# Kernel tuning notes

Measured on AMD Instinct MI355X. Metric: run time of the kernel, lower is better.

Reference implementation:

```python
import jax, jax.numpy as jnp
import numpy as np

IN_DIM, MEM_DIM, NUM_WORDS, N_LEAVES = 300, 256, 50000, 8192


def setup_inputs() -> dict:
    key = jax.random.key(0)
    ks = jax.random.split(key, 6)
    s = 0.05
    return {
        "embs": jax.random.normal(ks[0], (N_LEAVES, IN_DIM), jnp.float32),
        "Wx": jax.random.normal(ks[1], (4 * MEM_DIM, IN_DIM), jnp.float32) * s,
        "bx": jax.random.normal(ks[2], (4 * MEM_DIM,), jnp.float32) * s,
        "Wl": jax.random.normal(ks[3], (5 * MEM_DIM, MEM_DIM), jnp.float32) * s,
        "Wr": jax.random.normal(ks[4], (5 * MEM_DIM, MEM_DIM), jnp.float32) * s,
        "emb_table": jax.random.normal(ks[5], (NUM_WORDS, IN_DIM), jnp.float32),
    }


def reference(embs, Wx, bx, Wl, Wr, emb_table):
    m = Wl.shape[1]

    # x-projection order along fused axis: [cx, ix, fx, ox]
    def proj_x(x):  # [B, in] -> [B, 4, m]
        return (x @ Wx.T + bx).reshape(x.shape[0], 4, m)

    # hidden-projection order: [u, i, lf, rf, o]
    def compose(xg, lc, lh, rc, rh):
        lg = (lh @ Wl.T).reshape(-1, 5, m)
        rg = (rh @ Wr.T).reshape(-1, 5, m)
        u = jnp.tanh(xg[:, 0] + lg[:, 0] + rg[:, 0])
        i = jax.nn.sigmoid(xg[:, 1] + lg[:, 1] + rg[:, 1])
        lf = jax.nn.sigmoid(xg[:, 2] + lg[:, 2] + rg[:, 2])  # fx shared
        rf = jax.nn.sigmoid(xg[:, 2] + lg[:, 3] + rg[:, 3])  # fx shared
        c = i * u + lf * lc + rf * rc
        o = jax.nn.sigmoid(xg[:, 3] + lg[:, 4] + rg[:, 4])
        h = o * jnp.tanh(c)
        return c, h

    # leaves: zero child states, per-leaf embedding inputs
    L = embs.shape[0]
    z = jnp.zeros((L, m), embs.dtype)
    c, h = compose(proj_x(embs), z, z, z, z)

    # internal nodes (PAD=True): input is word_embedding(num_words - 1)
    pad_xg = proj_x(emb_table[-1:])  # [1, 4, m]

    while c.shape[0] > 1:  # static shapes; 13 merge levels
        lc, rc = c[0::2], c[1::2]
        lh, rh = h[0::2], h[1::2]
        B = lc.shape[0]
        c, h = compose(jnp.broadcast_to(pad_xg, (B, 4, m)), lc, lh, rc, rh)

    return jnp.stack([c, h])  # root (c, h): [2, 1, mem_dim]
```

## Files before the change

### kernel.cpp

```cpp
#include <hip/hip_runtime.h>
#include <math.h>


#define MEM 256

typedef __attribute__((ext_vector_type(8))) short bf16x8;
typedef __attribute__((ext_vector_type(4))) float f32x4;

__device__ __forceinline__ float sigf(float x) { return 1.0f / (1.0f + __expf(-x)); }

__device__ __forceinline__ unsigned short f2b(float f) {
  unsigned int u = __float_as_uint(f);
  u = (u + 0x7FFFu + ((u >> 16) & 1u)) >> 16;
  return (unsigned short)u;
}

__device__ __forceinline__ bf16x8 c8(const float* __restrict__ p) {
  float4 f0 = *(const float4*)(p);
  float4 f1 = *(const float4*)(p + 4);
  bf16x8 r;
  r[0] = (short)f2b(f0.x); r[1] = (short)f2b(f0.y);
  r[2] = (short)f2b(f0.z); r[3] = (short)f2b(f0.w);
  r[4] = (short)f2b(f1.x); r[5] = (short)f2b(f1.y);
  r[6] = (short)f2b(f1.z); r[7] = (short)f2b(f1.w);
  return r;
}

__device__ __forceinline__ bf16x8 g8(const float* __restrict__ rp, int k0) {
  if (k0 + 8 <= 300) return c8(rp + k0);
  bf16x8 r;
#pragma unroll
  for (int j = 0; j < 8; j++) {
    int k = k0 + j;
    r[j] = (k < 300) ? (short)f2b(rp[k]) : (short)0;
  }
  return r;
}

#define NB_EB 1280
#define NB_WCF 320
#define NB_WXF 120
__global__ __launch_bounds__(256) void k_prep(
    const float* __restrict__ embs, const float* __restrict__ Wx,
    const float* __restrict__ bx, const float* __restrict__ Wl,
    const float* __restrict__ Wr, const float* __restrict__ emb_last,
    unsigned short* __restrict__ eb, unsigned short* __restrict__ Wcf,
    unsigned short* __restrict__ Wxf, float* __restrict__ bias5) {
  int b = blockIdx.x, tid = threadIdx.x;
  if (b < NB_EB) {
    int idx8 = (b * 256 + tid) * 8;
    int row = idx8 / 320;
    int k0 = idx8 - row * 320;
    *(bf16x8*)(eb + idx8) = g8(embs + row * 300, k0);
  } else if (b < NB_EB + NB_WCF) {
    int idx8 = ((b - NB_EB) * 256 + tid) * 8;
    int f = idx8 >> 9, rr = idx8 & 511;
    int lane = rr >> 3;
    int gate = f % 5, t = f / 5;
    int grp = t & 15, kc = t >> 4;
    int k0 = kc * 32 + ((lane >> 4) << 3);
    int n = gate * 256 + (grp << 4) + (lane & 15);
    const float* src = (k0 < 256) ? (Wl + n * 256 + k0) : (Wr + n * 256 + (k0 - 256));
    *(bf16x8*)(Wcf + idx8) = c8(src);
  } else if (b < NB_EB + NB_WCF + NB_WXF) {
    int idx8 = ((b - NB_EB - NB_WCF) * 256 + tid) * 8;
    int f = idx8 >> 9, rr = idx8 & 511;
    int lane = rr >> 3;
    int gate = f % 3, t = f / 3;
    int grp = t & 15, kc = t >> 4;
    int k0 = kc * 32 + ((lane >> 4) << 3);
    const int gmap[3] = {0, 1, 3};
    int n = gmap[gate] * 256 + (grp << 4) + (lane & 15);
    *(bf16x8*)(Wxf + idx8) = g8(Wx + n * 300, k0);
  } else {
    int g = b - (NB_EB + NB_WCF + NB_WXF);
    __shared__ float er[300];
    for (int k = tid; k < 300; k += 256) er[k] = emb_last[k];
    __syncthreads();
    const int map[5] = {0, 1, 2, 2, 3};
    int wrow = map[g] * 256 + tid;
    const float* w = Wx + wrow * 300;
    float s = bx[wrow];
    for (int k = 0; k < 300; k++) s += er[k] * w[k];
    bias5[g * 256 + tid] = s;
  }
}

__global__ __launch_bounds__(256) void k_leaf_mfma(
    const unsigned short* __restrict__ eb, const unsigned short* __restrict__ Wxf,
    const float* __restrict__ bx, float* __restrict__ cO,
    unsigned short* __restrict__ hO) {
  int bid = blockIdx.x;
  int slice = bid & 7, rest = bid >> 3;
  int rowblock = slice * 8 + (rest & 7);
  int grp = rest >> 3;
  int lane = threadIdx.x & 63;
  int wave = threadIdx.x >> 6;
  int tb = (rowblock * 4 + wave) * 2;
  int m = lane & 15, quad = lane >> 4;

  f32x4 acc[2][3];
#pragma unroll
  for (int rt = 0; rt < 2; rt++)
#pragma unroll
    for (int g = 0; g < 3; g++) acc[rt][g] = (f32x4){0.f, 0.f, 0.f, 0.f};

  const unsigned short* ar0 = eb + (tb * 16 + m) * 320 + quad * 8;
  const unsigned short* ar1 = eb + ((tb + 1) * 16 + m) * 320 + quad * 8;
#pragma unroll
  for (int kc = 0; kc < 10; kc++) {
    const unsigned short* bp = Wxf + ((kc * 16 + grp) * 3) * 512 + lane * 8;
    bf16x8 b0 = *(const bf16x8*)(bp);
    bf16x8 b1 = *(const bf16x8*)(bp + 512);
    bf16x8 b2 = *(const bf16x8*)(bp + 1024);
    bf16x8 a0 = *(const bf16x8*)(ar0 + kc * 32);
    bf16x8 a1 = *(const bf16x8*)(ar1 + kc * 32);
    acc[0][0] = __builtin_amdgcn_mfma_f32_16x16x32_bf16(a0, b0, acc[0][0], 0, 0, 0);
    acc[0][1] = __builtin_amdgcn_mfma_f32_16x16x32_bf16(a0, b1, acc[0][1], 0, 0, 0);
    acc[0][2] = __builtin_amdgcn_mfma_f32_16x16x32_bf16(a0, b2, acc[0][2], 0, 0, 0);
    acc[1][0] = __builtin_amdgcn_mfma_f32_16x16x32_bf16(a1, b0, acc[1][0], 0, 0, 0);
    acc[1][1] = __builtin_amdgcn_mfma_f32_16x16x32_bf16(a1, b1, acc[1][1], 0, 0, 0);
    acc[1][2] = __builtin_amdgcn_mfma_f32_16x16x32_bf16(a1, b2, acc[1][2], 0, 0, 0);
  }
  int col = grp * 16 + m;
  float b0 = bx[col], b1 = bx[256 + col], b3 = bx[768 + col];
#pragma unroll
  for (int rt = 0; rt < 2; rt++) {
#pragma unroll
    for (int reg = 0; reg < 4; reg++) {
      int row = (tb + rt) * 16 + quad * 4 + reg;
      float u = tanhf(acc[rt][0][reg] + b0);
      float ig = sigf(acc[rt][1][reg] + b1);
      float o = sigf(acc[rt][2][reg] + b3);
      float c = ig * u;
      cO[row * MEM + col] = c;
      hO[row * MEM + col] = f2b(o * tanhf(c));
    }
  }
}

template <int RT>
__global__ __launch_bounds__(256) void k_compose_mfma(
    const unsigned short* __restrict__ hprev,
    const float* __restrict__ cprev,
    const unsigned short* __restrict__ Wcf, const float* __restrict__ bias5,
    float* __restrict__ cO, unsigned short* __restrict__ hO,
    float* __restrict__ hOf, int B) {
  int tiles = B >> 4;
  int gx = tiles / (4 * RT);
  int S = gx >= 8 ? 8 : gx;
  int pc = gx / S;
  int bid = blockIdx.x;
  int slice = bid % S;
  int rest = bid / S;
  int rowblock = slice * pc + rest % pc;
  int grp = rest / pc;
  int lane = threadIdx.x & 63;
  int wave = threadIdx.x >> 6;
  int tb = (rowblock * 4 + wave) * RT;
  if (tb * 16 >= B) return;
  int m = lane & 15, quad = lane >> 4;
  const bf16x8 zz = {0, 0, 0, 0, 0, 0, 0, 0};

  f32x4 acc[RT][5];
  const unsigned short* ar[RT];
  bool ok[RT];
#pragma unroll
  for (int rt = 0; rt < RT; rt++) {
    int ra = (tb + rt) * 16 + m;
    ok[rt] = (ra < B);
    ar[rt] = hprev + ra * 512 + quad * 8;
#pragma unroll
    for (int g = 0; g < 5; g++) acc[rt][g] = (f32x4){0.f, 0.f, 0.f, 0.f};
  }

#pragma unroll
  for (int kc = 0; kc < 16; kc++) {
    const unsigned short* bp = Wcf + ((kc * 16 + grp) * 5) * 512 + lane * 8;
    bf16x8 b0 = *(const bf16x8*)(bp);
    bf16x8 b1 = *(const bf16x8*)(bp + 512);
    bf16x8 b2 = *(const bf16x8*)(bp + 1024);
    bf16x8 b3 = *(const bf16x8*)(bp + 1536);
    bf16x8 b4 = *(const bf16x8*)(bp + 2048);
#pragma unroll
    for (int rt = 0; rt < RT; rt++) {
      bf16x8 a = ok[rt] ? *(const bf16x8*)(ar[rt] + kc * 32) : zz;
      acc[rt][0] = __builtin_amdgcn_mfma_f32_16x16x32_bf16(a, b0, acc[rt][0], 0, 0, 0);
      acc[rt][1] = __builtin_amdgcn_mfma_f32_16x16x32_bf16(a, b1, acc[rt][1], 0, 0, 0);
      acc[rt][2] = __builtin_amdgcn_mfma_f32_16x16x32_bf16(a, b2, acc[rt][2], 0, 0, 0);
      acc[rt][3] = __builtin_amdgcn_mfma_f32_16x16x32_bf16(a, b3, acc[rt][3], 0, 0, 0);
      acc[rt][4] = __builtin_amdgcn_mfma_f32_16x16x32_bf16(a, b4, acc[rt][4], 0, 0, 0);
    }
  }
  int col = grp * 16 + m;
  float b0 = bias5[col], b1 = bias5[256 + col], b2 = bias5[512 + col];
  float b3 = bias5[768 + col], b4 = bias5[1024 + col];
#pragma unroll
  for (int rt = 0; rt < RT; rt++) {
#pragma unroll
    for (int reg = 0; reg < 4; reg++) {
      int row = (tb + rt) * 16 + quad * 4 + reg;
      if (row >= B) continue;
      float u = tanhf(acc[rt][0][reg] + b0);
      float ig = sigf(acc[rt][1][reg] + b1);
      float lf = sigf(acc[rt][2][reg] + b2);
      float rf = sigf(acc[rt][3][reg] + b3);
      float o = sigf(acc[rt][4][reg] + b4);
      float lc = cprev[(2 * row) * MEM + col];
      float rc = cprev[(2 * row + 1) * MEM + col];
      float c = ig * u + lf * lc + rf * rc;
      float h = o * tanhf(c);
      cO[row * MEM + col] = c;
      hO[row * MEM + col] = f2b(h);
      if (hOf) hOf[row * MEM + col] = h;
    }
  }
}

__global__ __launch_bounds__(256) void k_compose_ksplit(
    const unsigned short* __restrict__ hprev, const float* __restrict__ cprev,
    const unsigned short* __restrict__ Wcf, const float* __restrict__ bias5,
    float* __restrict__ cO, unsigned short* __restrict__ hO,
    float* __restrict__ hOf, int B) {
  __shared__ __align__(16) float lds[4 * 2 * 5 * 64 * 4];
  int tid = threadIdx.x;
  int lane = tid & 63, wave = tid >> 6;
  int grp = blockIdx.y;
  int m = lane & 15, quad = lane >> 4;
  int tiles = (B + 15) >> 4;
  const bf16x8 zz = {0, 0, 0, 0, 0, 0, 0, 0};

  f32x4 acc[2][5];
  bool ok[2];
  const unsigned short* ar[2];
#pragma unroll
  for (int t = 0; t < 2; t++) {
    int ra = t * 16 + m;
    ok[t] = (t < tiles) && (ra < B);
    ar[t] = hprev + ra * 512 + quad * 8;
#pragma unroll
    for (int q = 0; q < 5; q++) acc[t][q] = (f32x4){0.f, 0.f, 0.f, 0.f};
  }

#pragma unroll
  for (int kcl = 0; kcl < 4; kcl++) {
    int kc = wave * 4 + kcl;
    const unsigned short* bp = Wcf + ((kc * 16 + grp) * 5) * 512 + lane * 8;
    bf16x8 b0 = *(const bf16x8*)(bp);
    bf16x8 b1 = *(const bf16x8*)(bp + 512);
    bf16x8 b2 = *(const bf16x8*)(bp + 1024);
    bf16x8 b3 = *(const bf16x8*)(bp + 1536);
    bf16x8 b4 = *(const bf16x8*)(bp + 2048);
#pragma unroll
    for (int t = 0; t < 2; t++) {
      if (t < tiles) {
        bf16x8 a = ok[t] ? *(const bf16x8*)(ar[t] + kc * 32) : zz;
        acc[t][0] = __builtin_amdgcn_mfma_f32_16x16x32_bf16(a, b0, acc[t][0], 0, 0, 0);
        acc[t][1] = __builtin_amdgcn_mfma_f32_16x16x32_bf16(a, b1, acc[t][1], 0, 0, 0);
        acc[t][2] = __builtin_amdgcn_mfma_f32_16x16x32_bf16(a, b2, acc[t][2], 0, 0, 0);
        acc[t][3] = __builtin_amdgcn_mfma_f32_16x16x32_bf16(a, b3, acc[t][3], 0, 0, 0);
        acc[t][4] = __builtin_amdgcn_mfma_f32_16x16x32_bf16(a, b4, acc[t][4], 0, 0, 0);
      }
    }
  }
#pragma unroll
  for (int t = 0; t < 2; t++)
    if (t < tiles)
#pragma unroll
      for (int q = 0; q < 5; q++)
        *(f32x4*)&lds[(((wave * 2 + t) * 5 + q) * 64 + lane) * 4] = acc[t][q];
  __syncthreads();

  if (wave < tiles) {
    int t = wave;
    int col = grp * 16 + m;
    float b0 = bias5[col], b1 = bias5[256 + col], b2 = bias5[512 + col];
    float b3 = bias5[768 + col], b4 = bias5[1024 + col];
    f32x4 s[5];
#pragma unroll
    for (int q = 0; q < 5; q++) {
      s[q] = *(const f32x4*)&lds[(((0 * 2 + t) * 5 + q) * 64 + lane) * 4];
#pragma unroll
      for (int v = 1; v < 4; v++) {
        f32x4 p = *(const f32x4*)&lds[(((v * 2 + t) * 5 + q) * 64 + lane) * 4];
        s[q][0] += p[0]; s[q][1] += p[1]; s[q][2] += p[2]; s[q][3] += p[3];
      }
    }
#pragma unroll
    for (int reg = 0; reg < 4; reg++) {
      int row = t * 16 + quad * 4 + reg;
      if (row >= B) continue;
      float u = tanhf(s[0][reg] + b0);
      float ig = sigf(s[1][reg] + b1);
      float lf = sigf(s[2][reg] + b2);
      float rf = sigf(s[3][reg] + b3);
      float o = sigf(s[4][reg] + b4);
      float lc = cprev[(2 * row) * MEM + col];
      float rc = cprev[(2 * row + 1) * MEM + col];
      float c = ig * u + lf * lc + rf * rc;
      float h = o * tanhf(c);
      cO[row * MEM + col] = c;
      hO[row * MEM + col] = f2b(h);
      if (hOf) hOf[row * MEM + col] = h;
    }
  }
}

extern "C" void kernel_launch(void* const* d_in, const int* in_sizes, int n_in,
                              void* d_out, int out_size, void* d_ws, size_t ws_size,
                              hipStream_t stream) {
  const float* embs = (const float*)d_in[0];
  const float* Wx = (const float*)d_in[1];
  const float* bx = (const float*)d_in[2];
  const float* Wl = (const float*)d_in[3];
  const float* Wr = (const float*)d_in[4];
  const float* emb_table = (const float*)d_in[5];
  float* out = (float*)d_out;

  float* ws = (float*)d_ws;
  float* cA = ws;
  float* cB = cA + 8192 * 256;
  float* bias5 = cB + 4096 * 256;
  unsigned short* hA = (unsigned short*)(bias5 + 1280);
  unsigned short* hB = hA + 8192 * 256;
  unsigned short* Wcf = hB + 4096 * 256;
  unsigned short* Wxf = Wcf + 1280 * 512;
  unsigned short* eb = Wxf + 480 * 512;

  k_prep<<<NB_EB + NB_WCF + NB_WXF + 5, 256, 0, stream>>>(
      embs, Wx, bx, Wl, Wr, emb_table + (in_sizes[5] - 300),
      eb, Wcf, Wxf, bias5);

  k_leaf_mfma<<<1024, 256, 0, stream>>>(eb, Wxf, bx, cA, hA);

  const float* cs = cA;
  const unsigned short* hs = hA;
  int B = 4096;
  int lvl = 0;
  while (B >= 1) {
    float* dc;
    unsigned short* dh;
    float* dhf = nullptr;
    if (B == 1) {
      dc = out;
      dh = hB;
      dhf = out + 256;
    } else if ((lvl & 1) == 0) {
      dc = cB; dh = hB;
    } else {
      dc = cA; dh = hA;
    }
    if (B == 4096) {
      int gx = (B >> 4) / 8;
      k_compose_mfma<2><<<gx * 16, 256, 0, stream>>>(
          hs, cs, Wcf, bias5, dc, dh, dhf, B);
    } else if (B >= 64) {
      int gx = (B >> 4) / 4;
      k_compose_mfma<1><<<gx * 16, 256, 0, stream>>>(
          hs, cs, Wcf, bias5, dc, dh, dhf, B);
    } else {
      k_compose_ksplit<<<dim3(1, 16), 256, 0, stream>>>(
          hs, cs, Wcf, bias5, dc, dh, dhf, B);
    }
    cs = dc;
    hs = dh;
    B >>= 1;
    lvl++;
  }
}
```

Measured before the change: 249.3 us.

## Fuse weight prep into leaf kernel and use K-split compose for all upper levels

Splits prep so that only the embedding and Wx conversion run before the leaf kernel. Wcf packing and the pad bias are moved into extra blocks of the leaf kernel, where they run alongside the leaf MFMA work. Every level from B=2048 down now uses the K-split compose kernel, with the A fragments preloaded into registers and tiles spread across blockIdx.x. This gives each block a quarter of K and so more blocks per level, at the cost of an LDS reduction step. The first level gets a dedicated RT=2 kernel with the bounds checks removed.

```diff
diff --git a/kernel.cpp b/kernel.cpp
--- a/kernel.cpp
+++ b/kernel.cpp
@@ -38,22 +38,87 @@
 }
 
 #define NB_EB 1280
-#define NB_WCF 320
 #define NB_WXF 120
-__global__ __launch_bounds__(256) void k_prep(
+__global__ __launch_bounds__(256) void k_prep1(
     const float* __restrict__ embs, const float* __restrict__ Wx,
-    const float* __restrict__ bx, const float* __restrict__ Wl,
-    const float* __restrict__ Wr, const float* __restrict__ emb_last,
-    unsigned short* __restrict__ eb, unsigned short* __restrict__ Wcf,
-    unsigned short* __restrict__ Wxf, float* __restrict__ bias5) {
+    unsigned short* __restrict__ eb, unsigned short* __restrict__ Wxf) {
   int b = blockIdx.x, tid = threadIdx.x;
   if (b < NB_EB) {
     int idx8 = (b * 256 + tid) * 8;
     int row = idx8 / 320;
     int k0 = idx8 - row * 320;
     *(bf16x8*)(eb + idx8) = g8(embs + row * 300, k0);
-  } else if (b < NB_EB + NB_WCF) {
+  } else {
     int idx8 = ((b - NB_EB) * 256 + tid) * 8;
+    int f = idx8 >> 9, rr = idx8 & 511;
+    int lane = rr >> 3;
+    int gate = f % 3, t = f / 3;
+    int grp = t & 15, kc = t >> 4;
+    int k0 = kc * 32 + ((lane >> 4) << 3);
+    const int gmap[3] = {0, 1, 3};
+    int n = gmap[gate] * 256 + (grp << 4) + (lane & 15);
+    *(bf16x8*)(Wxf + idx8) = g8(Wx + n * 300, k0);
+  }
+}
+
+#define NB_LEAF 1024
+#define NB_WCF 320
+__global__ __launch_bounds__(256) void k_leaf_fused(
+    const unsigned short* __restrict__ eb, const unsigned short* __restrict__ Wxf,
+    const float* __restrict__ bx, const float* __restrict__ Wx,
+    const float* __restrict__ Wl, const float* __restrict__ Wr,
+    const float* __restrict__ emb_last,
+    unsigned short* __restrict__ Wcf, float* __restrict__ bias5,
+    float* __restrict__ cO, unsigned short* __restrict__ hO) {
+  int b = blockIdx.x, tid = threadIdx.x;
+  if (b < NB_LEAF) {
+    int slice = b & 7, rest = b >> 3;
+    int rowblock = slice * 8 + (rest & 7);
+    int grp = rest >> 3;
+    int lane = tid & 63, wave = tid >> 6;
+    int tb = (rowblock * 4 + wave) * 2;
+    int m = lane & 15, quad = lane >> 4;
+
+    f32x4 acc[2][3];
+#pragma unroll
+    for (int rt = 0; rt < 2; rt++)
+#pragma unroll
+      for (int g = 0; g < 3; g++) acc[rt][g] = (f32x4){0.f, 0.f, 0.f, 0.f};
+
+    const unsigned short* ar0 = eb + (tb * 16 + m) * 320 + quad * 8;
+    const unsigned short* ar1 = eb + ((tb + 1) * 16 + m) * 320 + quad * 8;
+#pragma unroll
+    for (int kc = 0; kc < 10; kc++) {
+      const unsigned short* bp = Wxf + ((kc * 16 + grp) * 3) * 512 + lane * 8;
+      bf16x8 b0 = *(const bf16x8*)(bp);
+      bf16x8 b1 = *(const bf16x8*)(bp + 512);
+      bf16x8 b2 = *(const bf16x8*)(bp + 1024);
+      bf16x8 a0 = *(const bf16x8*)(ar0 + kc * 32);
+      bf16x8 a1 = *(const bf16x8*)(ar1 + kc * 32);
+      acc[0][0] = __builtin_amdgcn_mfma_f32_16x16x32_bf16(a0, b0, acc[0][0], 0, 0, 0);
+      acc[0][1] = __builtin_amdgcn_mfma_f32_16x16x32_bf16(a0, b1, acc[0][1], 0, 0, 0);
+      acc[0][2] = __builtin_amdgcn_mfma_f32_16x16x32_bf16(a0, b2, acc[0][2], 0, 0, 0);
+      acc[1][0] = __builtin_amdgcn_mfma_f32_16x16x32_bf16(a1, b0, acc[1][0], 0, 0, 0);
+      acc[1][1] = __builtin_amdgcn_mfma_f32_16x16x32_bf16(a1, b1, acc[1][1], 0, 0, 0);
+      acc[1][2] = __builtin_amdgcn_mfma_f32_16x16x32_bf16(a1, b2, acc[1][2], 0, 0, 0);
+    }
+    int col = grp * 16 + m;
+    float b0 = bx[col], b1 = bx[256 + col], b3 = bx[768 + col];
+#pragma unroll
+    for (int rt = 0; rt < 2; rt++) {
+#pragma unroll
+      for (int reg = 0; reg < 4; reg++) {
+        int row = (tb + rt) * 16 + quad * 4 + reg;
+        float u = tanhf(acc[rt][0][reg] + b0);
+        float ig = sigf(acc[rt][1][reg] + b1);
+        float o = sigf(acc[rt][2][reg] + b3);
+        float c = ig * u;
+        cO[row * MEM + col] = c;
+        hO[row * MEM + col] = f2b(o * tanhf(c));
+      }
+    }
+  } else if (b < NB_LEAF + NB_WCF) {
+    int idx8 = ((b - NB_LEAF) * 256 + tid) * 8;
     int f = idx8 >> 9, rr = idx8 & 511;
     int lane = rr >> 3;
     int gate = f % 5, t = f / 5;
@@ -62,18 +127,8 @@
     int n = gate * 256 + (grp << 4) + (lane & 15);
     const float* src = (k0 < 256) ? (Wl + n * 256 + k0) : (Wr + n * 256 + (k0 - 256));
     *(bf16x8*)(Wcf + idx8) = c8(src);
-  } else if (b < NB_EB + NB_WCF + NB_WXF) {
-    int idx8 = ((b - NB_EB - NB_WCF) * 256 + tid) * 8;
-    int f = idx8 >> 9, rr = idx8 & 511;
-    int lane = rr >> 3;
-    int gate = f % 3, t = f / 3;
-    int grp = t & 15, kc = t >> 4;
-    int k0 = kc * 32 + ((lane >> 4) << 3);
-    const int gmap[3] = {0, 1, 3};
-    int n = gmap[gate] * 256 + (grp << 4) + (lane & 15);
-    *(bf16x8*)(Wxf + idx8) = g8(Wx + n * 300, k0);
   } else {
-    int g = b - (NB_EB + NB_WCF + NB_WXF);
+    int g = b - (NB_LEAF + NB_WCF);
     __shared__ float er[300];
     for (int k = tid; k < 300; k += 256) er[k] = emb_last[k];
     __syncthreads();
@@ -86,89 +141,25 @@
   }
 }
 
-__global__ __launch_bounds__(256) void k_leaf_mfma(
-    const unsigned short* __restrict__ eb, const unsigned short* __restrict__ Wxf,
-    const float* __restrict__ bx, float* __restrict__ cO,
-    unsigned short* __restrict__ hO) {
+__global__ __launch_bounds__(256) void k_compose_rt2(
+    const unsigned short* __restrict__ hprev, const float* __restrict__ cprev,
+    const unsigned short* __restrict__ Wcf, const float* __restrict__ bias5,
+    float* __restrict__ cO, unsigned short* __restrict__ hO, int B) {
   int bid = blockIdx.x;
-  int slice = bid & 7, rest = bid >> 3;
-  int rowblock = slice * 8 + (rest & 7);
-  int grp = rest >> 3;
+  int slice = bid & 7;
+  int rest = bid >> 3;
+  int rowblock = slice * 4 + (rest & 3);
+  int grp = rest >> 2;
   int lane = threadIdx.x & 63;
   int wave = threadIdx.x >> 6;
   int tb = (rowblock * 4 + wave) * 2;
   int m = lane & 15, quad = lane >> 4;
 
-  f32x4 acc[2][3];
-#pragma unroll
-  for (int rt = 0; rt < 2; rt++)
-#pragma unroll
-    for (int g = 0; g < 3; g++) acc[rt][g] = (f32x4){0.f, 0.f, 0.f, 0.f};
-
-  const unsigned short* ar0 = eb + (tb * 16 + m) * 320 + quad * 8;
-  const unsigned short* ar1 = eb + ((tb + 1) * 16 + m) * 320 + quad * 8;
-#pragma unroll
-  for (int kc = 0; kc < 10; kc++) {
-    const unsigned short* bp = Wxf + ((kc * 16 + grp) * 3) * 512 + lane * 8;
-    bf16x8 b0 = *(const bf16x8*)(bp);
-    bf16x8 b1 = *(const bf16x8*)(bp + 512);
-    bf16x8 b2 = *(const bf16x8*)(bp + 1024);
-    bf16x8 a0 = *(const bf16x8*)(ar0 + kc * 32);
-    bf16x8 a1 = *(const bf16x8*)(ar1 + kc * 32);
-    acc[0][0] = __builtin_amdgcn_mfma_f32_16x16x32_bf16(a0, b0, acc[0][0], 0, 0, 0);
-    acc[0][1] = __builtin_amdgcn_mfma_f32_16x16x32_bf16(a0, b1, acc[0][1], 0, 0, 0);
-    acc[0][2] = __builtin_amdgcn_mfma_f32_16x16x32_bf16(a0, b2, acc[0][2], 0, 0, 0);
-    acc[1][0] = __builtin_amdgcn_mfma_f32_16x16x32_bf16(a1, b0, acc[1][0], 0, 0, 0);
-    acc[1][1] = __builtin_amdgcn_mfma_f32_16x16x32_bf16(a1, b1, acc[1][1], 0, 0, 0);
-    acc[1][2] = __builtin_amdgcn_mfma_f32_16x16x32_bf16(a1, b2, acc[1][2], 0, 0, 0);
-  }
-  int col = grp * 16 + m;
-  float b0 = bx[col], b1 = bx[256 + col], b3 = bx[768 + col];
+  f32x4 acc[2][5];
+  const unsigned short* ar[2];
 #pragma unroll
   for (int rt = 0; rt < 2; rt++) {
-#pragma unroll
-    for (int reg = 0; reg < 4; reg++) {
-      int row = (tb + rt) * 16 + quad * 4 + reg;
-      float u = tanhf(acc[rt][0][reg] + b0);
-      float ig = sigf(acc[rt][1][reg] + b1);
-      float o = sigf(acc[rt][2][reg] + b3);
-      float c = ig * u;
-      cO[row * MEM + col] = c;
-      hO[row * MEM + col] = f2b(o * tanhf(c));
-    }
-  }
-}
-
-template <int RT>
-__global__ __launch_bounds__(256) void k_compose_mfma(
-    const unsigned short* __restrict__ hprev,
-    const float* __restrict__ cprev,
-    const unsigned short* __restrict__ Wcf, const float* __restrict__ bias5,
-    float* __restrict__ cO, unsigned short* __restrict__ hO,
-    float* __restrict__ hOf, int B) {
-  int tiles = B >> 4;
-  int gx = tiles / (4 * RT);
-  int S = gx >= 8 ? 8 : gx;
-  int pc = gx / S;
-  int bid = blockIdx.x;
-  int slice = bid % S;
-  int rest = bid / S;
-  int rowblock = slice * pc + rest % pc;
-  int grp = rest / pc;
-  int lane = threadIdx.x & 63;
-  int wave = threadIdx.x >> 6;
-  int tb = (rowblock * 4 + wave) * RT;
-  if (tb * 16 >= B) return;
-  int m = lane & 15, quad = lane >> 4;
-  const bf16x8 zz = {0, 0, 0, 0, 0, 0, 0, 0};
-
-  f32x4 acc[RT][5];
-  const unsigned short* ar[RT];
-  bool ok[RT];
-#pragma unroll
-  for (int rt = 0; rt < RT; rt++) {
     int ra = (tb + rt) * 16 + m;
-    ok[rt] = (ra < B);
     ar[rt] = hprev + ra * 512 + quad * 8;
 #pragma unroll
     for (int g = 0; g < 5; g++) acc[rt][g] = (f32x4){0.f, 0.f, 0.f, 0.f};
@@ -183,8 +174,8 @@
     bf16x8 b3 = *(const bf16x8*)(bp + 1536);
     bf16x8 b4 = *(const bf16x8*)(bp + 2048);
 #pragma unroll
-    for (int rt = 0; rt < RT; rt++) {
-      bf16x8 a = ok[rt] ? *(const bf16x8*)(ar[rt] + kc * 32) : zz;
+    for (int rt = 0; rt < 2; rt++) {
+      bf16x8 a = *(const bf16x8*)(ar[rt] + kc * 32);
       acc[rt][0] = __builtin_amdgcn_mfma_f32_16x16x32_bf16(a, b0, acc[rt][0], 0, 0, 0);
       acc[rt][1] = __builtin_amdgcn_mfma_f32_16x16x32_bf16(a, b1, acc[rt][1], 0, 0, 0);
       acc[rt][2] = __builtin_amdgcn_mfma_f32_16x16x32_bf16(a, b2, acc[rt][2], 0, 0, 0);
@@ -196,11 +187,10 @@
   float b0 = bias5[col], b1 = bias5[256 + col], b2 = bias5[512 + col];
   float b3 = bias5[768 + col], b4 = bias5[1024 + col];
 #pragma unroll
-  for (int rt = 0; rt < RT; rt++) {
+  for (int rt = 0; rt < 2; rt++) {
 #pragma unroll
     for (int reg = 0; reg < 4; reg++) {
       int row = (tb + rt) * 16 + quad * 4 + reg;
-      if (row >= B) continue;
       float u = tanhf(acc[rt][0][reg] + b0);
       float ig = sigf(acc[rt][1][reg] + b1);
       float lf = sigf(acc[rt][2][reg] + b2);
@@ -209,15 +199,13 @@
       float lc = cprev[(2 * row) * MEM + col];
       float rc = cprev[(2 * row + 1) * MEM + col];
       float c = ig * u + lf * lc + rf * rc;
-      float h = o * tanhf(c);
       cO[row * MEM + col] = c;
-      hO[row * MEM + col] = f2b(h);
-      if (hOf) hOf[row * MEM + col] = h;
-    }
-  }
-}
-
-__global__ __launch_bounds__(256) void k_compose_ksplit(
+      hO[row * MEM + col] = f2b(o * tanhf(c));
+    }
+  }
+}
+
+__global__ __launch_bounds__(256, 4) void k_compose_ksplit(
     const unsigned short* __restrict__ hprev, const float* __restrict__ cprev,
     const unsigned short* __restrict__ Wcf, const float* __restrict__ bias5,
     float* __restrict__ cO, unsigned short* __restrict__ hO,
@@ -226,18 +214,24 @@
   int tid = threadIdx.x;
   int lane = tid & 63, wave = tid >> 6;
   int grp = blockIdx.y;
+  int tp = blockIdx.x;
   int m = lane & 15, quad = lane >> 4;
   int tiles = (B + 15) >> 4;
   const bf16x8 zz = {0, 0, 0, 0, 0, 0, 0, 0};
 
   f32x4 acc[2][5];
-  bool ok[2];
-  const unsigned short* ar[2];
+  bool act[2], ok[2];
+  bf16x8 av[2][4];
 #pragma unroll
   for (int t = 0; t < 2; t++) {
-    int ra = t * 16 + m;
-    ok[t] = (t < tiles) && (ra < B);
-    ar[t] = hprev + ra * 512 + quad * 8;
+    int gt = 2 * tp + t;
+    act[t] = (gt < tiles);
+    int ra = gt * 16 + m;
+    ok[t] = act[t] && (ra < B);
+    const unsigned short* ar = hprev + ra * 512 + quad * 8;
+#pragma unroll
+    for (int kcl = 0; kcl < 4; kcl++)
+      av[t][kcl] = ok[t] ? *(const bf16x8*)(ar + (wave * 4 + kcl) * 32) : zz;
 #pragma unroll
     for (int q = 0; q < 5; q++) acc[t][q] = (f32x4){0.f, 0.f, 0.f, 0.f};
   }
@@ -253,26 +247,26 @@
     bf16x8 b4 = *(const bf16x8*)(bp + 2048);
 #pragma unroll
     for (int t = 0; t < 2; t++) {
-      if (t < tiles) {
-        bf16x8 a = ok[t] ? *(const bf16x8*)(ar[t] + kc * 32) : zz;
-        acc[t][0] = __builtin_amdgcn_mfma_f32_16x16x32_bf16(a, b0, acc[t][0], 0, 0, 0);
-        acc[t][1] = __builtin_amdgcn_mfma_f32_16x16x32_bf16(a, b1, acc[t][1], 0, 0, 0);
-        acc[t][2] = __builtin_amdgcn_mfma_f32_16x16x32_bf16(a, b2, acc[t][2], 0, 0, 0);
-        acc[t][3] = __builtin_amdgcn_mfma_f32_16x16x32_bf16(a, b3, acc[t][3], 0, 0, 0);
-        acc[t][4] = __builtin_amdgcn_mfma_f32_16x16x32_bf16(a, b4, acc[t][4], 0, 0, 0);
+      if (act[t]) {
+        acc[t][0] = __builtin_amdgcn_mfma_f32_16x16x32_bf16(av[t][kcl], b0, acc[t][0], 0, 0, 0);
+        acc[t][1] = __builtin_amdgcn_mfma_f32_16x16x32_bf16(av[t][kcl], b1, acc[t][1], 0, 0, 0);
+        acc[t][2] = __builtin_amdgcn_mfma_f32_16x16x32_bf16(av[t][kcl], b2, acc[t][2], 0, 0, 0);
+        acc[t][3] = __builtin_amdgcn_mfma_f32_16x16x32_bf16(av[t][kcl], b3, acc[t][3], 0, 0, 0);
+        acc[t][4] = __builtin_amdgcn_mfma_f32_16x16x32_bf16(av[t][kcl], b4, acc[t][4], 0, 0, 0);
       }
     }
   }
 #pragma unroll
   for (int t = 0; t < 2; t++)
-    if (t < tiles)
+    if (act[t])
 #pragma unroll
       for (int q = 0; q < 5; q++)
         *(f32x4*)&lds[(((wave * 2 + t) * 5 + q) * 64 + lane) * 4] = acc[t][q];
   __syncthreads();
 
-  if (wave < tiles) {
+  if (wave < 2 && act[wave]) {
     int t = wave;
+    int gt = 2 * tp + t;
     int col = grp * 16 + m;
     float b0 = bias5[col], b1 = bias5[256 + col], b2 = bias5[512 + col];
     float b3 = bias5[768 + col], b4 = bias5[1024 + col];
@@ -288,7 +282,7 @@
     }
 #pragma unroll
     for (int reg = 0; reg < 4; reg++) {
-      int row = t * 16 + quad * 4 + reg;
+      int row = gt * 16 + quad * 4 + reg;
       if (row >= B) continue;
       float u = tanhf(s[0][reg] + b0);
       float ig = sigf(s[1][reg] + b1);
@@ -327,41 +321,35 @@
   unsigned short* Wxf = Wcf + 1280 * 512;
   unsigned short* eb = Wxf + 480 * 512;
 
-  k_prep<<<NB_EB + NB_WCF + NB_WXF + 5, 256, 0, stream>>>(
-      embs, Wx, bx, Wl, Wr, emb_table + (in_sizes[5] - 300),
-      eb, Wcf, Wxf, bias5);
-
-  k_leaf_mfma<<<1024, 256, 0, stream>>>(eb, Wxf, bx, cA, hA);
-
-  const float* cs = cA;
-  const unsigned short* hs = hA;
-  int B = 4096;
-  int lvl = 0;
+  k_prep1<<<NB_EB + NB_WXF, 256, 0, stream>>>(embs, Wx, eb, Wxf);
+
+  k_leaf_fused<<<NB_LEAF + NB_WCF + 5, 256, 0, stream>>>(
+      eb, Wxf, bx, Wx, Wl, Wr, emb_table + (in_sizes[5] - 300),
+      Wcf, bias5, cA, hA);
+
+  k_compose_rt2<<<512, 256, 0, stream>>>(hA, cA, Wcf, bias5, cB, hB, 4096);
+
+  const float* cs = cB;
+  const unsigned short* hs = hB;
+  int B = 2048;
+  int lvl = 1;
   while (B >= 1) {
     float* dc;
     unsigned short* dh;
     float* dhf = nullptr;
     if (B == 1) {
       dc = out;
-      dh = hB;
+      dh = hA;
       dhf = out + 256;
     } else if ((lvl & 1) == 0) {
       dc = cB; dh = hB;
     } else {
       dc = cA; dh = hA;
     }
-    if (B == 4096) {
-      int gx = (B >> 4) / 8;
-      k_compose_mfma<2><<<gx * 16, 256, 0, stream>>>(
-          hs, cs, Wcf, bias5, dc, dh, dhf, B);
-    } else if (B >= 64) {
-      int gx = (B >> 4) / 4;
-      k_compose_mfma<1><<<gx * 16, 256, 0, stream>>>(
-          hs, cs, Wcf, bias5, dc, dh, dhf, B);
-    } else {
-      k_compose_ksplit<<<dim3(1, 16), 256, 0, stream>>>(
-          hs, cs, Wcf, bias5, dc, dh, dhf, B);
-    }
+    int tiles = (B + 15) / 16;
+    int gx = (tiles + 1) / 2;
+    k_compose_ksplit<<<dim3(gx, 16), 256, 0, stream>>>(
+        hs, cs, Wcf, bias5, dc, dh, dhf, B);
     cs = dc;
     hs = dh;
     B >>= 1;
```

After: 227.6 us. -8.7%, faster.
